# Kernel tuning notes

Hardware: AMD Instinct MI355X
Metric: run time of the kernel (lower is better)

Reference implementation:

```python
import jax, jax.numpy as jnp
import numpy as np

NE, EW, TOP_K, T_D, MAXNNZ = 32, 2944, 4, 8, 256
ALPHA, LIMIT, ORIG = 1.702, 7.0, 2880
HID = 2048


def setup_inputs() -> dict:
    key = jax.random.key(0)
    ks = jax.random.split(key, 7)
    dt = jnp.float16
    hid = jax.random.normal(ks[0], (1, 1024, HID), dtype=dt)
    # rand_init() sets all params to torch.rand(...)/5 -> Uniform[0, 0.2)
    gate_w = (jax.random.uniform(ks[1], (NE, HID), dtype=dt) * 0.2).astype(dt)
    u = (jax.random.uniform(ks[2], (NE * EW, HID), dtype=dt) * 0.2).astype(dt)
    g = (jax.random.uniform(ks[3], (NE * EW, HID), dtype=dt) * 0.2).astype(dt)
    d = (jax.random.uniform(ks[4], (HID, NE * EW), dtype=dt) * 0.2).astype(dt)
    ub = (jax.random.uniform(ks[5], (NE * EW,), dtype=dt) * 0.2).astype(dt)
    gb = (jax.random.uniform(ks[6], (NE * EW,), dtype=dt) * 0.2).astype(dt)
    return {"hid": hid, "gate_w": gate_w, "u": u, "g": g, "d": d, "ub": ub, "gb": gb}


def _act(up, gate):
    # clamped GLU: gate clamped above, up clamped both sides; glu = g*sigmoid(alpha*g); (up+1)*glu
    gate = jnp.minimum(gate, LIMIT)
    up = jnp.clip(up, -LIMIT, LIMIT)
    glu = gate * jax.nn.sigmoid(gate * ALPHA)
    act = (up + 1.0) * glu
    return act.at[..., ORIG:].set(0)  # padded inter dims (2880..2944) zeroed


def _forward(hid, gate_w, u, g, d, ub, gb):
    B, S, H = hid.shape
    x = hid.reshape(-1, H)           # [bs, H]
    bs = x.shape[0]

    # --- routing: softmax -> top-k -> renormalize -> scatter to sparse weights ---
    logits = (x @ gate_w.T).astype(jnp.float32)          # [bs, NE]
    probs = jax.nn.softmax(logits, axis=1)
    vals, idx = jax.lax.top_k(probs, TOP_K)
    vals = vals / vals.sum(axis=1, keepdims=True)
    sparse_rw = jnp.zeros_like(probs).at[jnp.arange(bs)[:, None], idx].set(vals)
    rw = sparse_rw.astype(x.dtype)                        # [bs, NE]

    # --- expert selection: t_d dense experts + t_d sparse experts by load ---
    routing_n = jnp.count_nonzero(rw, axis=0)
    mask_c = jax.lax.top_k(routing_n, 2 * T_D)[1]         # [2*T_D]
    cd, cs = mask_c[:T_D], mask_c[T_D:]
    # top-MAXNNZ tokens per sparse expert
    mask_r = jax.lax.top_k(sparse_rw[:, cs].T, MAXNNZ)[1].T  # [MAXNNZ, T_D]

    U = u.reshape(NE, EW, H)
    G = g.reshape(NE, EW, H)
    UB = ub.reshape(NE, EW)
    GB = gb.reshape(NE, EW)
    D = d.reshape(H, NE, EW)

    # --- dense experts: every token runs through the t_d hottest experts ---
    up_d = jnp.einsum('nh,teh->nte', x, U[cd]) + UB[cd]   # [bs, T_D, EW]
    gt_d = jnp.einsum('nh,teh->nte', x, G[cd]) + GB[cd]
    act_d = _act(up_d, gt_d) * rw[:, cd][..., None]       # routing weight combine
    out = jnp.einsum('nte,hte->nh', act_d, D[:, cd])      # [bs, H]

    # --- sparse experts: gather top-MAXNNZ tokens, MLP, scatter-add back ---
    xs = x[mask_r]                                        # [M, T_D, H]
    up_s = jnp.einsum('mth,teh->mte', xs, U[cs]) + UB[cs]
    gt_s = jnp.einsum('mth,teh->mte', xs, G[cs]) + GB[cs]
    w_s = rw[mask_r, cs[None, :]]                         # [M, T_D]
    act_s = _act(up_s, gt_s) * w_s[..., None]
    contrib = jnp.einsum('mte,hte->mth', act_s, D[:, cs])  # [M, T_D, H]
    out = out.at[mask_r.reshape(-1)].add(contrib.reshape(-1, H))

    return out.reshape(B, S, H)


def reference(hid, gate_w, u, g, d, ub, gb):
    return _forward(hid, gate_w, u, g, d, ub, gb)
```

## Files before the change

### kernel.cpp

```cpp
#include <hip/hip_runtime.h>

#define HID 2048
#define NE_ 32
#define EW_ 2944
#define ORIG_ 2880
#define TOPK_ 4
#define MAXNNZ_ 256
#define BS_ 1024
#define NEWTOT (NE_*EW_)

typedef unsigned short u16;
typedef _Float16 h8  __attribute__((ext_vector_type(8)));
typedef float  f32x4 __attribute__((ext_vector_type(4)));
typedef float  fv4   __attribute__((ext_vector_type(4)));

__device__ __forceinline__ u16 f2h_bits(float f){
  union{ _Float16 h; u16 u; } c; c.h = (_Float16)f; return c.u;
}
__device__ __forceinline__ float f16q(float f){ return (float)(_Float16)f; }

__device__ __forceinline__ h8 cvt8(fv4 a, fv4 b){
  h8 r;
  r[0]=(_Float16)a[0]; r[1]=(_Float16)a[1]; r[2]=(_Float16)a[2]; r[3]=(_Float16)a[3];
  r[4]=(_Float16)b[0]; r[5]=(_Float16)b[1]; r[6]=(_Float16)b[2]; r[7]=(_Float16)b[3];
  return r;
}
__device__ __forceinline__ int ldsx(int row, int chunk){
  return row*32 + ((chunk ^ ((row>>1)&3))*8);
}

__device__ __forceinline__ void barrier_lgkm(){
  asm volatile("s_waitcnt lgkmcnt(0)" ::: "memory");
  __builtin_amdgcn_s_barrier();
  __builtin_amdgcn_sched_barrier(0);
}

__device__ __forceinline__ int rank_kth(const int* counts, int kth){
  int cnt[NE_]; bool used[NE_];
  for (int e=0;e<NE_;e++){ cnt[e]=counts[e]; used[e]=false; }
  int bi=0;
  for (int k=0;k<=kth;k++){
    int best=-1; bi=0;
    for (int e=0;e<NE_;e++) if(!used[e] && cnt[e]>best){best=cnt[e];bi=e;}
    used[bi]=true;
  }
  return bi;
}

__global__ __launch_bounds__(256) void k_gate(const float* __restrict__ x,
                                              const float* __restrict__ gw,
                                              float* __restrict__ rw,
                                              float* __restrict__ rwf,
                                              int* __restrict__ counts,
                                              u16* __restrict__ xh)
{
  __shared__ float slog[4][NE_];
  const int tid = threadIdx.x, wid = tid>>6, lane = tid&63;
  const int n = blockIdx.x*4 + wid;
  const float* xr = x + (size_t)n*HID + lane*32;
  float xf[32];
  #pragma unroll
  for (int i=0;i<8;i++){
    fv4 v = *(const fv4*)(xr + i*4);
    #pragma unroll
    for (int j=0;j<4;j++) xf[i*4+j] = v[j];
  }
  #pragma unroll
  for (int c=0;c<4;c++){
    h8 hv;
    #pragma unroll
    for (int j=0;j<8;j++) hv[j] = (_Float16)xf[c*8+j];
    *(h8*)(xh + (size_t)n*HID + lane*32 + c*8) = hv;
  }
  for (int e=0;e<NE_;e++){
    const float* gr = gw + (size_t)e*HID + lane*32;
    float p = 0.f;
    #pragma unroll
    for (int i=0;i<8;i++){
      fv4 v = *(const fv4*)(gr + i*4);
      #pragma unroll
      for (int j=0;j<4;j++) p += xf[i*4+j]*v[j];
    }
    #pragma unroll
    for (int s=32;s>0;s>>=1) p += __shfl_xor(p, s);
    if (lane==0) slog[wid][e] = f16q(p);
  }
  if (lane==0){
    float mx=-1e30f;
    for (int e=0;e<NE_;e++) mx = fmaxf(mx, slog[wid][e]);
    float pr[NE_]; float sum=0.f;
    for (int e=0;e<NE_;e++){ float v=__expf(slog[wid][e]-mx); pr[e]=v; sum+=v; }
    for (int e=0;e<NE_;e++) pr[e] = pr[e]/sum;
    int   idx[TOPK_]; float val[TOPK_]; bool used[NE_];
    for (int e=0;e<NE_;e++) used[e]=false;
    float vs=0.f;
    for (int k=0;k<TOPK_;k++){
      float best=-1.f; int bi=0;
      for (int e=0;e<NE_;e++) if(!used[e] && pr[e]>best){best=pr[e];bi=e;}
      used[bi]=true; idx[k]=bi; val[k]=best; vs+=best;
    }
    float* rwr  = rw  + (size_t)n*NE_;
    float* rwfr = rwf + (size_t)n*NE_;
    for (int k=0;k<TOPK_;k++){
      float vraw = val[k]/vs;
      float q = f16q(vraw);
      rwr[idx[k]]  = q;
      rwfr[idx[k]] = vraw;
      if (q!=0.f) atomicAdd(counts+idx[k], 1);
    }
  }
}

__global__ __launch_bounds__(256) void k_lists(const float* __restrict__ rw,
                                               const float* __restrict__ rwf,
                                               const int* __restrict__ counts,
                                               int* __restrict__ cdcs,
                                               int* __restrict__ tok_all,
                                               int* __restrict__ cnt_all,
                                               int* __restrict__ inv,
                                               int* __restrict__ invcnt)
{
  __shared__ float v[BS_];
  __shared__ int scnt;
  __shared__ int e_sh;
  const int z = blockIdx.x;
  const int tid = threadIdx.x;
  if (tid==0){
    int e = rank_kth(counts, z);
    e_sh = e;
    cdcs[z] = e;
    scnt = 0;
  }
  for (int i=tid;i<BS_;i+=256) tok_all[z*BS_+i] = 0;
  __syncthreads();
  const int e = e_sh;
  for (int i=tid;i<BS_;i+=256) v[i] = (z<8) ? rw[(size_t)i*NE_+e] : rwf[(size_t)i*NE_+e];
  __syncthreads();
  for (int i=tid;i<BS_;i+=256){
    bool take;
    if (z<8){
      take = (v[i]!=0.f);
    } else {
      float vi=v[i]; int r=0;
      for (int m=0;m<BS_;m++){
        float vm=v[m];
        r += (vm>vi) || (vm==vi && m<i);
      }
      take = (r<MAXNNZ_) && (rw[(size_t)i*NE_+e]!=0.f);
    }
    if (take){
      int slot = atomicAdd(&scnt,1);
      tok_all[z*BS_+slot] = i;
      int c = atomicAdd(&invcnt[i],1);
      inv[i*4+c] = (z<<16) | slot;
    }
  }
  __syncthreads();
  if (tid==0) cnt_all[z] = scnt;
}

#define FSTEP(P, KT)                                                        \
{                                                                           \
  u16* A = ldsA[(P)&1]; u16* B = ldsB[(P)&1];                               \
  _Pragma("unroll")                                                         \
  for (int r=0;r<4;r++) *(h8*)&A[ldsx(ar + r*64, ach)] = Aset[(P)&1][r];    \
  *(h8*)&B[ldsx(br, ach)] = cvt8(Bsa[(P)], Bsb[(P)]);                       \
  if ((KT)+2 < NKF){                                                        \
    const int k2 = ((KT)+2)*32;                                             \
    _Pragma("unroll")                                                       \
    for (int r=0;r<4;r++) Aset[(P)&1][r] = *(const h8*)(ap[r]+k2);          \
  }                                                                         \
  if ((KT)+4 < NKF){                                                        \
    const int k4 = ((KT)+4)*32;                                             \
    Bsa[(P)] = *(const fv4*)(bp+k4); Bsb[(P)] = *(const fv4*)(bp+k4+4);     \
  }                                                                         \
  barrier_lgkm();                                                           \
  h8 af[4], fu[2], fg[2];                                                   \
  _Pragma("unroll")                                                         \
  for (int m=0;m<4;m++) af[m] = *(const h8*)&A[ldsx(w*64+m*16+lr, kq)];     \
  _Pragma("unroll")                                                         \
  for (int n2=0;n2<2;n2++){                                                 \
    fu[n2] = *(const h8*)&B[ldsx(   n2*16+lr, kq)];                         \
    fg[n2] = *(const h8*)&B[ldsx(32+n2*16+lr, kq)];                         \
  }                                                                         \
  _Pragma("unroll")                                                         \
  for (int m=0;m<4;m++)                                                     \
    _Pragma("unroll")                                                       \
    for (int n2=0;n2<2;n2++){                                               \
      au[m][n2]=__builtin_amdgcn_mfma_f32_16x16x32_f16(af[m],fu[n2],au[m][n2],0,0,0); \
      ag[m][n2]=__builtin_amdgcn_mfma_f32_16x16x32_f16(af[m],fg[n2],ag[m][n2],0,0,0); \
    }                                                                       \
}

__global__ __launch_bounds__(256, 2) void k_fused(const u16* __restrict__ xh,
                                               const float* __restrict__ uw,
                                               const float* __restrict__ gww,
                                               const float* __restrict__ ub,
                                               const float* __restrict__ gb,
                                               const float* __restrict__ rw,
                                               const int* __restrict__ cdcs,
                                               const int* __restrict__ tok_all,
                                               const int* __restrict__ cnt_all,
                                               u16* __restrict__ act)
{
  const int z=blockIdx.z, bx=blockIdx.x, by=blockIdx.y;
  const int cnt = cnt_all[z];
  if (by*256 >= cnt) return;
  const int e = cdcs[z];
  __shared__ __align__(16) u16 ldsA[2][256*32];
  __shared__ __align__(16) u16 ldsB[2][64*32];
  const int tid=threadIdx.x, lane=tid&63, w=tid>>6;
  const int lr = lane&15, kq = lane>>4;
  const int ar = tid>>2, ach = tid&3;
  const u16* ap[4];
  #pragma unroll
  for (int r=0;r<4;r++){
    const int tok = tok_all[z*BS_ + by*256 + ar + r*64];
    ap[r] = xh + (size_t)tok*HID + ach*8;
  }
  const int br = ar;
  const float* bp = (br<32 ? uw  + ((size_t)e*EW_ + bx*32 + br)*HID
                           : gww + ((size_t)e*EW_ + bx*32 + (br-32))*HID) + ach*8;

  f32x4 au[4][2], ag[4][2];
  #pragma unroll
  for (int i=0;i<4;i++)
    #pragma unroll
    for (int j=0;j<2;j++)
      #pragma unroll
      for (int q=0;q<4;q++){ au[i][j][q]=0.f; ag[i][j][q]=0.f; }

  h8 Aset[2][4]; fv4 Bsa[4], Bsb[4];
  #pragma unroll
  for (int r=0;r<4;r++){
    Aset[0][r] = *(const h8*)ap[r];
    Aset[1][r] = *(const h8*)(ap[r]+32);
  }
  #pragma unroll
  for (int p=0;p<4;p++){
    Bsa[p] = *(const fv4*)(bp+p*32); Bsb[p] = *(const fv4*)(bp+p*32+4);
  }

  const int NKF = HID/32;
  for (int kt=0; kt<NKF; kt+=4){
    FSTEP(0, kt)
    FSTEP(1, kt+1)
    FSTEP(2, kt+2)
    FSTEP(3, kt+3)
  }

  #pragma unroll
  for (int n2=0;n2<2;n2++){
    const int col = bx*32 + n2*16 + lr;
    const float ubv = ub[(size_t)e*EW_ + col];
    const float gbv = gb[(size_t)e*EW_ + col];
    #pragma unroll
    for (int m=0;m<4;m++){
      #pragma unroll
      for (int j=0;j<4;j++){
        const int s = by*256 + w*64 + m*16 + kq*4 + j;
        if (s < cnt){
          float upv = f16q(au[m][n2][j] + ubv);
          float gtv = f16q(ag[m][n2][j] + gbv);
          float wv = rw[(size_t)tok_all[z*BS_+s]*NE_ + e];
          float gc = fminf(gtv, 7.0f);
          float uc = fminf(fmaxf(upv,-7.0f),7.0f);
          float glu = gc * (1.f/(1.f+__expf(-gc*1.702f)));
          act[((size_t)z*BS_+s)*ORIG_ + col] = f2h_bits((uc+1.f)*glu*wv);
        }
      }
    }
  }
}

#define DSTEP(P, KT)                                                        \
{                                                                           \
  u16* A = ldsA[(P)&1]; u16* B = ldsB[(P)&1];                               \
  _Pragma("unroll")                                                         \
  for (int r=0;r<4;r++) *(h8*)&A[ldsx(ar + r*64, ach)] = Aset[(P)&1][r];    \
  *(h8*)&B[ldsx(br, ach)] = cvt8(Bsa[(P)], Bsb[(P)]);                       \
  if ((KT)+2 < NKD){                                                        \
    const int k2 = ((KT)+2)*32;                                             \
    _Pragma("unroll")                                                       \
    for (int r=0;r<4;r++) Aset[(P)&1][r] = *(const h8*)(ap[r]+k2);          \
  }                                                                         \
  if ((KT)+4 < NKD){                                                        \
    const int k4 = ((KT)+4)*32;                                             \
    Bsa[(P)] = *(const fv4*)(bp+k4); Bsb[(P)] = *(const fv4*)(bp+k4+4);     \
  }                                                                         \
  barrier_lgkm();                                                           \
  h8 af[4], bfr[4];                                                         \
  _Pragma("unroll")                                                         \
  for (int m=0;m<4;m++)    af[m]  = *(const h8*)&A[ldsx(w*64+m*16+lr, kq)]; \
  _Pragma("unroll")                                                         \
  for (int n2=0;n2<4;n2++) bfr[n2] = *(const h8*)&B[ldsx(n2*16+lr, kq)];    \
  _Pragma("unroll")                                                         \
  for (int m=0;m<4;m++)                                                     \
    _Pragma("unroll")                                                       \
    for (int n2=0;n2<4;n2++)                                                \
      acc[m][n2]=__builtin_amdgcn_mfma_f32_16x16x32_f16(af[m],bfr[n2],acc[m][n2],0,0,0); \
}

__global__ __launch_bounds__(256, 2) void k_down(const u16* __restrict__ act,
                                              const float* __restrict__ dw,
                                              const int* __restrict__ cdcs,
                                              const int* __restrict__ cnt_all,
                                              u16* __restrict__ contrib)
{
  const int zz=blockIdx.z, bx=blockIdx.x, by=blockIdx.y;
  const int z = zz>>1, kh = zz&1;
  const int cnt = cnt_all[z];
  if (by*256 >= cnt) return;
  const int e = cdcs[z];
  __shared__ __align__(16) u16 ldsA[2][256*32];
  __shared__ __align__(16) u16 ldsB[2][64*32];
  const int tid=threadIdx.x, lane=tid&63, w=tid>>6;
  const int lr = lane&15, kq = lane>>4;
  const int ar = tid>>2, ach = tid&3;
  const int kbase = kh*1440;

  const u16* ap[4];
  #pragma unroll
  for (int r=0;r<4;r++)
    ap[r] = act + ((size_t)z*BS_ + by*256 + ar + r*64)*ORIG_ + kbase + ach*8;
  const int br = ar;
  const float* bp = dw + (size_t)(bx*64 + br)*NEWTOT + (size_t)e*EW_ + kbase + ach*8;

  f32x4 acc[4][4];
  #pragma unroll
  for (int i=0;i<4;i++)
    #pragma unroll
    for (int j=0;j<4;j++)
      #pragma unroll
      for (int q=0;q<4;q++) acc[i][j][q]=0.f;

  h8 Aset[2][4]; fv4 Bsa[4], Bsb[4];
  #pragma unroll
  for (int r=0;r<4;r++){
    Aset[0][r] = *(const h8*)ap[r];
    Aset[1][r] = *(const h8*)(ap[r]+32);
  }
  #pragma unroll
  for (int p=0;p<4;p++){
    Bsa[p] = *(const fv4*)(bp+p*32); Bsb[p] = *(const fv4*)(bp+p*32+4);
  }

  const int NKD = 1440/32;
  for (int kt=0; kt<44; kt+=4){
    DSTEP(0, kt)
    DSTEP(1, kt+1)
    DSTEP(2, kt+2)
    DSTEP(3, kt+3)
  }
  DSTEP(0, 44)

  #pragma unroll
  for (int m=0;m<4;m++){
    #pragma unroll
    for (int j=0;j<4;j++){
      const int slot = by*256 + w*64 + m*16 + kq*4 + j;
      if (slot < cnt){
        #pragma unroll
        for (int n2=0;n2<4;n2++){
          const int col = bx*64 + n2*16 + lr;
          contrib[((size_t)zz*BS_ + slot)*HID + col] = f2h_bits(acc[m][n2][j]);
        }
      }
    }
  }
}

__global__ __launch_bounds__(256) void k_combine(const u16* __restrict__ contrib,
                                                 const int* __restrict__ inv,
                                                 const int* __restrict__ invcnt,
                                                 float* __restrict__ out)
{
  const int gid = blockIdx.x*256 + threadIdx.x;
  const int base = gid*8;
  const int n = base >> 11;
  const int h = base & 2047;
  float acc[8];
  #pragma unroll
  for (int q=0;q<8;q++) acc[q]=0.f;
  const int c = invcnt[n];
  for (int j=0;j<c;j++){
    const int code = inv[n*4+j];
    const int z = code>>16;
    const int slot = code & 0xFFFF;
    const u16* p = contrib + ((size_t)(z*2)*BS_ + slot)*HID + h;
    h8 v0 = *(const h8*)p;
    h8 v1 = *(const h8*)(p + (size_t)BS_*HID);
    #pragma unroll
    for (int q=0;q<8;q++) acc[q] += (float)v0[q] + (float)v1[q];
  }
  fv4 o0, o1;
  #pragma unroll
  for (int q=0;q<4;q++){ o0[q]=acc[q]; o1[q]=acc[4+q]; }
  *(fv4*)(out + base) = o0;
  *(fv4*)(out + base + 4) = o1;
}

extern "C" void kernel_launch(void* const* d_in, const int* in_sizes, int n_in,
                              void* d_out, int out_size, void* d_ws, size_t ws_size,
                              hipStream_t stream)
{
  const float* x  = (const float*)d_in[0];
  const float* gw = (const float*)d_in[1];
  const float* u  = (const float*)d_in[2];
  const float* g  = (const float*)d_in[3];
  const float* dw = (const float*)d_in[4];
  const float* ub = (const float*)d_in[5];
  const float* gb = (const float*)d_in[6];

  char* ws = (char*)d_ws;
  size_t off = 0;
  auto alloc = [&](size_t bytes)->void*{ void* p = ws + off; off += (bytes + 255) & ~(size_t)255; return p; };
  float* rw     = (float*)alloc((size_t)BS_*NE_*4);
  float* rwf    = (float*)alloc((size_t)BS_*NE_*4);
  int*   counts = (int*)  alloc(NE_*4);
  int*   invcnt = (int*)  alloc(BS_*4);
  size_t zero_span = off;
  int*   cdcs   = (int*)  alloc(16*4);
  int*   cnt_all= (int*)  alloc(16*4);
  int*   tok_all= (int*)  alloc((size_t)16*BS_*4);
  int*   inv    = (int*)  alloc((size_t)BS_*4*4);
  u16*   xh     = (u16*)  alloc((size_t)BS_*HID*2);
  u16*   act    = (u16*)  alloc((size_t)16*BS_*ORIG_*2);
  u16*   contrib= (u16*)  alloc((size_t)32*BS_*HID*2);
  if (off > ws_size) return;

  hipMemsetAsync(ws, 0, zero_span, stream);

  k_gate <<<BS_/4, 256, 0, stream>>>(x, gw, rw, rwf, counts, xh);
  k_lists<<<16,    256, 0, stream>>>(rw, rwf, counts, cdcs, tok_all, cnt_all, inv, invcnt);

  k_fused<<<dim3(ORIG_/32, 4, 16), 256, 0, stream>>>(xh, u, g, ub, gb, rw,
                                                     cdcs, tok_all, cnt_all, act);
  k_down <<<dim3(HID/64, 4, 32), 256, 0, stream>>>(act, dw, cdcs, cnt_all, contrib);
  k_combine<<<BS_*HID/(256*8), 256, 0, stream>>>(contrib, inv, invcnt, (float*)d_out);
}
```

Before: 567.8 us.

## Load fp32 up/gate weights in contiguous 128-wide K chunks with wider LDS tile

Each thread now loads 32 contiguous fp32 weight values, a full 128-byte segment, every 4 K-steps. Previously it loaded two strided 16-byte vectors per step. The B tile in LDS grows to 64x128 halves, double-buffered per 128-K chunk, with a new XOR swizzle. The intent is better-coalesced, longer global bursts for the weight stream and less per-step load overhead. The cost is more registers (8 fv4) and more LDS, which may hurt the 2-blocks-per-CU occupancy.

Result: slower. 586.5 us (+3.3%).

```diff
diff --git a/kernel.cpp b/kernel.cpp
--- a/kernel.cpp
+++ b/kernel.cpp
@@ -27,6 +27,9 @@
 }
 __device__ __forceinline__ int ldsx(int row, int chunk){
   return row*32 + ((chunk ^ ((row>>1)&3))*8);
+}
+__device__ __forceinline__ int ldsxB(int row, int chunk){
+  return row*128 + ((chunk ^ (row&15))*8);
 }
 
 __device__ __forceinline__ void barrier_lgkm(){
@@ -159,29 +162,39 @@
   if (tid==0) cnt_all[z] = scnt;
 }
 
-#define FSTEP(P, KT)                                                        \
+#define FSTEP3(I, KK4)                                                      \
 {                                                                           \
-  u16* A = ldsA[(P)&1]; u16* B = ldsB[(P)&1];                               \
-  _Pragma("unroll")                                                         \
-  for (int r=0;r<4;r++) *(h8*)&A[ldsx(ar + r*64, ach)] = Aset[(P)&1][r];    \
-  *(h8*)&B[ldsx(br, ach)] = cvt8(Bsa[(P)], Bsb[(P)]);                       \
-  if ((KT)+2 < NKF){                                                        \
-    const int k2 = ((KT)+2)*32;                                             \
+  const int kk = (KK4) + (I);                                               \
+  u16* A = ldsA[(I)&1];                                                     \
+  _Pragma("unroll")                                                         \
+  for (int r=0;r<4;r++) *(h8*)&A[ldsx(ar + r*64, ach)] = Aset[(I)&1][r];    \
+  if ((I)==0){                                                              \
+    const int ko = (KK4)>>2;                                                \
+    u16* B = ldsB[ko&1];                                                    \
     _Pragma("unroll")                                                       \
-    for (int r=0;r<4;r++) Aset[(P)&1][r] = *(const h8*)(ap[r]+k2);          \
+    for (int c=0;c<4;c++)                                                   \
+      *(h8*)&B[ldsxB(br, seg*4+c)] = cvt8(Breg[2*c], Breg[2*c+1]);          \
+    if (ko+1<16){                                                           \
+      const float* bsrc = bp + (ko+1)*128;                                  \
+      _Pragma("unroll")                                                     \
+      for (int c=0;c<8;c++) Breg[c] = *(const fv4*)(bsrc + c*4);            \
+    }                                                                       \
   }                                                                         \
-  if ((KT)+4 < NKF){                                                        \
-    const int k4 = ((KT)+4)*32;                                             \
-    Bsa[(P)] = *(const fv4*)(bp+k4); Bsb[(P)] = *(const fv4*)(bp+k4+4);     \
+  if (kk+2<64){                                                             \
+    const int k2 = (kk+2)*32;                                               \
+    _Pragma("unroll")                                                       \
+    for (int r=0;r<4;r++) Aset[(I)&1][r] = *(const h8*)(ap[r]+k2);          \
   }                                                                         \
   barrier_lgkm();                                                           \
+  const u16* Bb = ldsB[((KK4)>>2)&1];                                       \
   h8 af[4], fu[2], fg[2];                                                   \
   _Pragma("unroll")                                                         \
   for (int m=0;m<4;m++) af[m] = *(const h8*)&A[ldsx(w*64+m*16+lr, kq)];     \
+  const int cb = ((I)&3)*4 + kq;                                            \
   _Pragma("unroll")                                                         \
   for (int n2=0;n2<2;n2++){                                                 \
-    fu[n2] = *(const h8*)&B[ldsx(   n2*16+lr, kq)];                         \
-    fg[n2] = *(const h8*)&B[ldsx(32+n2*16+lr, kq)];                         \
+    fu[n2] = *(const h8*)&Bb[ldsxB(   n2*16+lr, cb)];                       \
+    fg[n2] = *(const h8*)&Bb[ldsxB(32+n2*16+lr, cb)];                       \
   }                                                                         \
   _Pragma("unroll")                                                         \
   for (int m=0;m<4;m++)                                                     \
@@ -208,7 +221,7 @@
   if (by*256 >= cnt) return;
   const int e = cdcs[z];
   __shared__ __align__(16) u16 ldsA[2][256*32];
-  __shared__ __align__(16) u16 ldsB[2][64*32];
+  __shared__ __align__(16) u16 ldsB[2][64*128];
   const int tid=threadIdx.x, lane=tid&63, w=tid>>6;
   const int lr = lane&15, kq = lane>>4;
   const int ar = tid>>2, ach = tid&3;
@@ -218,9 +231,9 @@
     const int tok = tok_all[z*BS_ + by*256 + ar + r*64];
     ap[r] = xh + (size_t)tok*HID + ach*8;
   }
-  const int br = ar;
+  const int br = tid>>2, seg = tid&3;
   const float* bp = (br<32 ? uw  + ((size_t)e*EW_ + bx*32 + br)*HID
-                           : gww + ((size_t)e*EW_ + bx*32 + (br-32))*HID) + ach*8;
+                           : gww + ((size_t)e*EW_ + bx*32 + (br-32))*HID) + seg*32;
 
   f32x4 au[4][2], ag[4][2];
   #pragma unroll
@@ -230,23 +243,20 @@
       #pragma unroll
       for (int q=0;q<4;q++){ au[i][j][q]=0.f; ag[i][j][q]=0.f; }
 
-  h8 Aset[2][4]; fv4 Bsa[4], Bsb[4];
+  h8 Aset[2][4]; fv4 Breg[8];
   #pragma unroll
   for (int r=0;r<4;r++){
     Aset[0][r] = *(const h8*)ap[r];
     Aset[1][r] = *(const h8*)(ap[r]+32);
   }
   #pragma unroll
-  for (int p=0;p<4;p++){
-    Bsa[p] = *(const fv4*)(bp+p*32); Bsb[p] = *(const fv4*)(bp+p*32+4);
-  }
-
-  const int NKF = HID/32;
-  for (int kt=0; kt<NKF; kt+=4){
-    FSTEP(0, kt)
-    FSTEP(1, kt+1)
-    FSTEP(2, kt+2)
-    FSTEP(3, kt+3)
+  for (int c=0;c<8;c++) Breg[c] = *(const fv4*)(bp + c*4);
+
+  for (int kk4=0; kk4<64; kk4+=4){
+    FSTEP3(0, kk4)
+    FSTEP3(1, kk4)
+    FSTEP3(2, kk4)
+    FSTEP3(3, kk4)
   }
 
   #pragma unroll
```
